# Kernel tuning notes

Hardware: AMD Instinct MI355X
Metric: run time of the kernel (lower is better)

Reference implementation:

```python
import jax, jax.numpy as jnp
import numpy as np

NEG_SLOPE = 0.1

def lrelu(x):
    return jnp.where(x >= 0, x, NEG_SLOPE * x)

def conv2d(x, w, b, padding=0, dilation=1):
    y = jax.lax.conv_general_dilated(
        x, w, window_strides=(1, 1),
        padding=[(padding, padding), (padding, padding)],
        rhs_dilation=(dilation, dilation),
        dimension_numbers=('NCHW', 'OIHW', 'NCHW'))
    return y + b[None, :, None, None]

def res_aspp(x, p):
    r1 = lrelu(conv2d(x, p['a1_w'], p['a1_b'], padding=1, dilation=1))
    r2 = lrelu(conv2d(x, p['a2_w'], p['a2_b'], padding=2, dilation=2))
    r3 = lrelu(conv2d(x, p['a3_w'], p['a3_b'], padding=4, dilation=4))
    r = conv2d(jnp.concatenate((r1, r2, r3), axis=1), p['ar_w'], p['ar_b'])
    return x + r

def deform_conv2d(x, offset, w, b):
    # x: [B,C,H,W], offset: [B,2*K,H,W] torchvision layout (y,x) per 3x3 tap
    B, C, H, W = x.shape
    KH = KW = 3
    K = KH * KW
    pad = 1
    off = offset.reshape(B, K, 2, H, W)
    ky, kx = jnp.meshgrid(jnp.arange(KH), jnp.arange(KW), indexing='ij')
    ky = ky.reshape(K).astype(x.dtype)
    kx = kx.reshape(K).astype(x.dtype)
    hh = jnp.arange(H, dtype=x.dtype)
    ww = jnp.arange(W, dtype=x.dtype)
    # sampling positions [B,K,H,W]
    py = off[:, :, 0] + (hh[None, None, :, None] - pad + ky[None, :, None, None])
    px = off[:, :, 1] + (ww[None, None, None, :] - pad + kx[None, :, None, None])
    y0 = jnp.floor(py)
    x0 = jnp.floor(px)
    wy = (py - y0)[:, None]  # [B,1,K,H,W]
    wx = (px - x0)[:, None]
    y0i = y0.astype(jnp.int32)
    x0i = x0.astype(jnp.int32)
    x_flat = x.reshape(B, C, H * W)

    def gather(iy, ix):
        valid = ((iy >= 0) & (iy < H) & (ix >= 0) & (ix < W)).astype(x.dtype)
        idx = jnp.clip(iy, 0, H - 1) * W + jnp.clip(ix, 0, W - 1)  # [B,K,H,W]
        v = jax.vmap(lambda xb, ib: xb[:, ib])(x_flat, idx.reshape(B, -1))
        return v.reshape(B, C, K, H, W) * valid[:, None]

    samp = (gather(y0i, x0i) * (1 - wy) * (1 - wx)
            + gather(y0i, x0i + 1) * (1 - wy) * wx
            + gather(y0i + 1, x0i) * wy * (1 - wx)
            + gather(y0i + 1, x0i + 1) * wy * wx)
    out = jnp.einsum('bckhw,ock->bohw', samp, w.reshape(w.shape[0], C, K))
    return out + b[None, :, None, None]

def setup_inputs() -> dict:
    key = jax.random.key(0)
    ks = jax.random.split(key, 16)
    B, C, H, W = 4, 64, 160, 160
    Cout = 64
    s = 0.05
    d = {
        'in_aux': jax.random.normal(ks[0], (B, C, H, W), jnp.float32),
        'in_ref': jax.random.normal(ks[1], (B, C, H, W), jnp.float32),
        'w01': jax.random.normal(ks[2], (Cout, 2 * C, 1, 1), jnp.float32) * s,
        'b01': jnp.zeros((Cout,), jnp.float32),
        'a1_w': jax.random.normal(ks[3], (Cout, Cout, 3, 3), jnp.float32) * s,
        'a1_b': jnp.zeros((Cout,), jnp.float32),
        'a2_w': jax.random.normal(ks[4], (Cout, Cout, 3, 3), jnp.float32) * s,
        'a2_b': jnp.zeros((Cout,), jnp.float32),
        'a3_w': jax.random.normal(ks[5], (Cout, Cout, 3, 3), jnp.float32) * s,
        'a3_b': jnp.zeros((Cout,), jnp.float32),
        'ar_w': jax.random.normal(ks[6], (Cout, 3 * Cout, 1, 1), jnp.float32) * s,
        'ar_b': jnp.zeros((Cout,), jnp.float32),
        'w02': jax.random.normal(ks[7], (18, Cout, 1, 1), jnp.float32) * s,
        'b02': jnp.zeros((18,), jnp.float32),
        'dw': jax.random.normal(ks[8], (Cout, C, 3, 3), jnp.float32) * s,
        'db': jnp.zeros((Cout,), jnp.float32),
    }
    return d

def reference(in_aux, in_ref, w01, b01, a1_w, a1_b, a2_w, a2_b, a3_w, a3_b,
              ar_w, ar_b, w02, b02, dw, db):
    cat_x = jnp.concatenate((in_aux, in_ref), axis=1)
    off_x = lrelu(conv2d(cat_x, w01, b01))
    p = {'a1_w': a1_w, 'a1_b': a1_b, 'a2_w': a2_w, 'a2_b': a2_b,
         'a3_w': a3_w, 'a3_b': a3_b, 'ar_w': ar_w, 'ar_b': ar_b}
    off_x = res_aspp(off_x, p)
    off_x = conv2d(off_x, w02, b02)
    return deform_conv2d(in_aux, off_x, dw, db)
```

## Files before the change

kernel.cpp:

```cpp
#include <hip/hip_runtime.h>
#include <math.h>

static constexpr int B = 4, H = 160, W = 160;
static constexpr int HW = H * W;
static constexpr int CHW = 64 * HW;
static constexpr int NELEM = B * CHW;

typedef short bf16x8 __attribute__((ext_vector_type(8)));
typedef float f32x4 __attribute__((ext_vector_type(4)));

__device__ __forceinline__ float lrelu(float v) { return v >= 0.f ? v : 0.1f * v; }

__device__ __forceinline__ unsigned short f2bf(float f) {
  unsigned u = __float_as_uint(f);
  return (unsigned short)((u + 0x7FFFu + ((u >> 16) & 1u)) >> 16);
}
__device__ __forceinline__ float bf2f(short u) {
  return __uint_as_float(((unsigned)(unsigned short)u) << 16);
}

__global__ __launch_bounds__(256) void k_transform(
    const float* __restrict__ w01, const float* __restrict__ dw,
    const float* __restrict__ arw, const float* __restrict__ a1w,
    const float* __restrict__ a2w, const float* __restrict__ a3w,
    float* __restrict__ wt01, unsigned short* __restrict__ wb_bf,
    unsigned short* __restrict__ wd_bf, unsigned short* __restrict__ arw_bf) {
  int i = blockIdx.x * 256 + threadIdx.x;
  if (i < 8192) {
    int ci = i >> 6, o = i & 63;
    wt01[i] = w01[o * 128 + ci];
  } else if (i < 118784) {
    int j = i - 8192;
    int ci = j & 63, co = (j >> 6) & 63;
    int kk = j >> 12;
    int dsel = kk / 9; kk -= dsel * 9;
    const float* src = dsel == 0 ? a1w : dsel == 1 ? a2w : a3w;
    wb_bf[j] = f2bf(src[(co * 64 + ci) * 9 + kk]);
  } else if (i < 155648) {
    int j = i - 118784;
    int ci = j & 63, co = (j >> 6) & 63, k = j >> 12;
    wd_bf[j] = f2bf(dw[(co * 64 + ci) * 9 + k]);
  } else if (i < 167936) {
    int j = i - 155648;
    arw_bf[j] = f2bf(arw[j]);
  }
}

__global__ __launch_bounds__(256) void k_conv1x1_in(
    const float* __restrict__ aux, const float* __restrict__ ref,
    const float* __restrict__ wt01, const float* __restrict__ b01,
    float* __restrict__ out, unsigned short* __restrict__ out_bf,
    unsigned short* __restrict__ x_bf) {
  __shared__ float s[128 * 64];
  int pos0 = blockIdx.x * 64;
  int b = pos0 / HW;
  int hw0 = pos0 - b * HW;
  int tid = threadIdx.x;
  for (int i = tid; i < 8192; i += 256) {
    int ci = i >> 6, p = i & 63;
    const float* src = (ci < 64) ? (aux + b * CHW + ci * HW)
                                 : (ref + b * CHW + (ci - 64) * HW);
    s[i] = src[hw0 + p];
  }
  __syncthreads();
  int p = tid & 63;
  int g = __builtin_amdgcn_readfirstlane(tid >> 6);
  const float* wp = wt01 + g * 16;
  float acc[16];
#pragma unroll
  for (int j = 0; j < 16; ++j) acc[j] = 0.f;
#pragma unroll 4
  for (int ci = 0; ci < 128; ++ci) {
    float sv = s[ci * 64 + p];
    const float* wrow = wp + ci * 64;
#pragma unroll
    for (int j = 0; j < 16; ++j) acc[j] += sv * wrow[j];
  }
  const float* bb = b01 + g * 16;
  int obase = (b * 64 + g * 16) * HW + hw0 + p;
  unsigned short tb[16];
#pragma unroll
  for (int j = 0; j < 16; ++j) {
    float v = lrelu(acc[j] + bb[j]);
    out[obase + j * HW] = v;
    tb[j] = f2bf(v);
  }
  unsigned short* dst = out_bf + ((size_t)(b * HW + hw0 + p)) * 64 + g * 16;
  *(uint4*)dst = *(const uint4*)&tb[0];
  *(uint4*)(dst + 8) = *(const uint4*)&tb[8];
  unsigned short xb[16];
#pragma unroll
  for (int j = 0; j < 16; ++j) xb[j] = f2bf(s[(g * 16 + j) * 64 + p]);
  unsigned short* xdst = x_bf + ((size_t)(b * HW + hw0 + p)) * 64 + g * 16;
  *(uint4*)xdst = *(const uint4*)&xb[0];
  *(uint4*)(xdst + 8) = *(const uint4*)&xb[8];
}

__global__ __launch_bounds__(256) void k_aspp3_mfma(
    const unsigned short* __restrict__ off0_bf,
    const unsigned short* __restrict__ wb_bf,
    const float* __restrict__ a1b, const float* __restrict__ a2b,
    const float* __restrict__ a3b, unsigned short* __restrict__ r_bf) {
  __shared__ unsigned short sin[576 * 40];
  int bx = blockIdx.x, by = blockIdx.y;
  int dsel = blockIdx.z >> 2, b = blockIdx.z & 3;
  int d = 1 << dsel;
  const float* bias = dsel == 0 ? a1b : dsel == 1 ? a2b : a3b;
  int tid = threadIdx.x;
  int lane = tid & 63, wid = tid >> 6;
  int m = lane & 15, q = lane >> 4;
  f32x4 acc[4][4] = {};
  const unsigned short* wbase = wb_bf + dsel * 9 * 4096;

  for (int ch = 0; ch < 2; ++ch) {
    __syncthreads();
    for (int i = tid; i < 2304; i += 256) {
      int pix = i >> 2, sub = i & 3;
      int py = pix / 24, px = pix - py * 24;
      int gy = by * 16 + py - 4, gx = bx * 16 + px - 4;
      uint4 v = make_uint4(0u, 0u, 0u, 0u);
      if (gy >= 0 && gy < H && gx >= 0 && gx < W)
        v = *(const uint4*)(off0_bf +
                            ((size_t)(b * HW + gy * W + gx)) * 64 + ch * 32 + sub * 8);
      *(uint4*)(sin + pix * 40 + sub * 8) = v;
    }
    __syncthreads();
#pragma unroll
    for (int k = 0; k < 9; ++k) {
      int ky = k / 3, kx = k - ky * 3;
      bf16x8 bfrag[4];
#pragma unroll
      for (int t = 0; t < 4; ++t)
        bfrag[t] = *(const bf16x8*)(wbase + ((k * 64 + t * 16 + m) * 64) + ch * 32 + q * 8);
      bf16x8 afrag[4];
#pragma unroll
      for (int mt = 0; mt < 4; ++mt) {
        int row = 4 + wid * 4 + mt + (ky - 1) * d;
        int col = 4 + m + (kx - 1) * d;
        afrag[mt] = *(const bf16x8*)(sin + (row * 24 + col) * 40 + q * 8);
      }
#pragma unroll
      for (int mt = 0; mt < 4; ++mt)
#pragma unroll
        for (int t = 0; t < 4; ++t)
          acc[mt][t] = __builtin_amdgcn_mfma_f32_16x16x32_bf16(
              afrag[mt], bfrag[t], acc[mt][t], 0, 0, 0);
    }
  }

  unsigned short* epb = sin;
  __syncthreads();
#pragma unroll
  for (int t = 0; t < 4; ++t) {
    float bi = bias[t * 16 + m];
#pragma unroll
    for (int mt = 0; mt < 4; ++mt) {
      int prow = wid * 4 + mt;
#pragma unroll
      for (int r = 0; r < 4; ++r) {
        int pix = prow * 16 + q * 4 + r;
        epb[pix * 72 + t * 16 + m] = f2bf(lrelu(acc[mt][t][r] + bi));
      }
    }
  }
  __syncthreads();
  {
    int pix = tid;
    int prow = pix >> 4, pcol = pix & 15;
    unsigned short* dst =
        r_bf + ((size_t)(b * HW + (by * 16 + prow) * W + bx * 16 + pcol)) * 192 +
        dsel * 64;
    const unsigned short* src = epb + pix * 72;
#pragma unroll
    for (int c = 0; c < 8; ++c)
      *(uint4*)(dst + c * 8) = *(const uint4*)(src + c * 8);
  }
}

__global__ __launch_bounds__(256) void k_merge_head_mfma(
    const unsigned short* __restrict__ r_bf, const float* __restrict__ off0,
    const unsigned short* __restrict__ arw_bf, const float* __restrict__ arb,
    const float* __restrict__ w02, const float* __restrict__ b02,
    float* __restrict__ offs) {
  __shared__ unsigned short sa[64 * 200];
  int pos0 = blockIdx.x * 64;
  int b = pos0 / HW;
  int hw0 = pos0 - b * HW;
  int tid = threadIdx.x;
  const unsigned short* gsrc = r_bf + (size_t)(b * HW + hw0) * 192;
  for (int i = tid; i < 1536; i += 256) {
    int pos = i / 24, c8 = i - pos * 24;
    *(uint4*)(sa + pos * 200 + c8 * 8) = *(const uint4*)(gsrc + i * 8);
  }
  __syncthreads();
  int lane = tid & 63, wid = tid >> 6;
  int m = lane & 15, q = lane >> 4;
  f32x4 acc[4] = {};
#pragma unroll
  for (int kc = 0; kc < 6; ++kc) {
    bf16x8 bfrag = *(const bf16x8*)(arw_bf + (wid * 16 + m) * 192 + kc * 32 + q * 8);
#pragma unroll
    for (int mt = 0; mt < 4; ++mt) {
      bf16x8 afrag = *(const bf16x8*)(sa + (mt * 16 + m) * 200 + kc * 32 + q * 8);
      acc[mt] = __builtin_amdgcn_mfma_f32_16x16x32_bf16(afrag, bfrag, acc[mt],
                                                        0, 0, 0);
    }
  }
  __syncthreads();
  float* ep = (float*)sa;
  int co = wid * 16 + m;
  float bi = arb[co];
  const float* resrow = off0 + (size_t)(b * 64 + co) * HW + hw0;
#pragma unroll
  for (int mt = 0; mt < 4; ++mt)
#pragma unroll
    for (int r = 0; r < 4; ++r) {
      int pos = mt * 16 + q * 4 + r;
      ep[pos * 65 + co] = acc[mt][r] + bi + resrow[pos];
    }
  __syncthreads();
  for (int i = tid; i < 1152; i += 256) {
    int t = i >> 6, p = i & 63;
    const float* w2 = w02 + t * 64;
    float o = b02[t];
#pragma unroll 8
    for (int c = 0; c < 64; ++c) o += ep[p * 65 + c] * w2[c];
    offs[(b * 18 + t) * HW + hw0 + p] = o;
  }
}

__global__ __launch_bounds__(256) void k_deform_mfma(
    const unsigned short* __restrict__ x_bf, const float* __restrict__ offs,
    const unsigned short* __restrict__ wd_bf, const float* __restrict__ db,
    float* __restrict__ out) {
  constexpr int SP = 72;
  __shared__ unsigned short sb[2][64 * SP];
  int blk = (blockIdx.x & 7) * 200 + (blockIdx.x >> 3);
  int pos0 = blk * 64;
  int b = pos0 / HW;
  int hw0 = pos0 - b * HW;
  int tid = threadIdx.x;
  int lane = tid & 63, wid = tid >> 6;
  int m = lane & 15, q = lane >> 4;
  int p = lane;
  int cg = wid;
  int hw = hw0 + p;
  int h = hw / W, wv = hw - h * W;
  const unsigned short* xb = x_bf + (size_t)b * HW * 64;
  const float* ob = offs + b * 18 * HW + hw;
  float offv[18];
#pragma unroll
  for (int j = 0; j < 18; ++j) offv[j] = ob[j * HW];
  f32x4 acc[4] = {};

#pragma unroll
  for (int k = 0; k < 9; ++k) {
    const int ky = k / 3, kx = k - ky * 3;
    float py = offv[2 * k] + (float)(h - 1 + ky);
    float px = offv[2 * k + 1] + (float)(wv - 1 + kx);
    float fy = floorf(py), fx = floorf(px);
    int iy0 = (int)fy, ix0 = (int)fx;
    float wy = py - fy, wx = px - fx;
    int iy1 = iy0 + 1, ix1 = ix0 + 1;
    float vy0 = (iy0 >= 0 && iy0 < H) ? 1.f : 0.f;
    float vy1 = (iy1 >= 0 && iy1 < H) ? 1.f : 0.f;
    float vx0 = (ix0 >= 0 && ix0 < W) ? 1.f : 0.f;
    float vx1 = (ix1 >= 0 && ix1 < W) ? 1.f : 0.f;
    int cy0 = min(max(iy0, 0), H - 1), cy1 = min(max(iy1, 0), H - 1);
    int cx0 = min(max(ix0, 0), W - 1), cx1 = min(max(ix1, 0), W - 1);
    float c00 = vy0 * vx0 * (1.f - wy) * (1.f - wx);
    float c01 = vy0 * vx1 * (1.f - wy) * wx;
    float c10 = vy1 * vx0 * wy * (1.f - wx);
    float c11 = vy1 * vx1 * wy * wx;
    const unsigned short* p00 = xb + (size_t)(cy0 * W + cx0) * 64 + cg * 16;
    const unsigned short* p01 = xb + (size_t)(cy0 * W + cx1) * 64 + cg * 16;
    const unsigned short* p10 = xb + (size_t)(cy1 * W + cx0) * 64 + cg * 16;
    const unsigned short* p11 = xb + (size_t)(cy1 * W + cx1) * 64 + cg * 16;
    unsigned short tb[16];
#pragma unroll
    for (int c2 = 0; c2 < 2; ++c2) {
      bf16x8 v00 = *(const bf16x8*)(p00 + c2 * 8);
      bf16x8 v01 = *(const bf16x8*)(p01 + c2 * 8);
      bf16x8 v10 = *(const bf16x8*)(p10 + c2 * 8);
      bf16x8 v11 = *(const bf16x8*)(p11 + c2 * 8);
#pragma unroll
      for (int j = 0; j < 8; ++j) {
        float sv = c00 * bf2f(v00[j]) + c01 * bf2f(v01[j]) +
                   c10 * bf2f(v10[j]) + c11 * bf2f(v11[j]);
        tb[c2 * 8 + j] = f2bf(sv);
      }
    }
    unsigned short* wr = &sb[k & 1][p * SP + cg * 16];
    *(uint4*)wr = *(const uint4*)&tb[0];
    *(uint4*)(wr + 8) = *(const uint4*)&tb[8];
    __syncthreads();
    const unsigned short* rb = &sb[k & 1][0];
#pragma unroll
    for (int kc = 0; kc < 2; ++kc) {
      bf16x8 bfrag =
          *(const bf16x8*)(wd_bf + (k * 64 + wid * 16 + m) * 64 + kc * 32 + q * 8);
#pragma unroll
      for (int mt = 0; mt < 4; ++mt) {
        bf16x8 afrag = *(const bf16x8*)(rb + (mt * 16 + m) * SP + kc * 32 + q * 8);
        acc[mt] = __builtin_amdgcn_mfma_f32_16x16x32_bf16(afrag, bfrag, acc[mt],
                                                          0, 0, 0);
      }
    }
  }
  int co = wid * 16 + m;
  float bias = db[co];
  size_t orow = (size_t)(b * 64 + co) * HW + hw0;
#pragma unroll
  for (int mt = 0; mt < 4; ++mt)
#pragma unroll
    for (int r = 0; r < 4; ++r)
      out[orow + mt * 16 + q * 4 + r] = acc[mt][r] + bias;
}

extern "C" void kernel_launch(void* const* d_in, const int* in_sizes, int n_in,
                              void* d_out, int out_size, void* d_ws, size_t ws_size,
                              hipStream_t stream) {
  const float* aux = (const float*)d_in[0];
  const float* ref = (const float*)d_in[1];
  const float* w01 = (const float*)d_in[2];
  const float* b01 = (const float*)d_in[3];
  const float* a1w = (const float*)d_in[4];
  const float* a1b = (const float*)d_in[5];
  const float* a2w = (const float*)d_in[6];
  const float* a2b = (const float*)d_in[7];
  const float* a3w = (const float*)d_in[8];
  const float* a3b = (const float*)d_in[9];
  const float* arw = (const float*)d_in[10];
  const float* arb = (const float*)d_in[11];
  const float* w02 = (const float*)d_in[12];
  const float* b02 = (const float*)d_in[13];
  const float* dw  = (const float*)d_in[14];
  const float* db  = (const float*)d_in[15];
  float* out = (float*)d_out;

  float* off0 = (float*)d_ws;
  float* offs = off0 + NELEM;
  float* wt01 = offs + B * 18 * HW;
  unsigned short* off0_bf = (unsigned short*)(wt01 + 8192);
  unsigned short* x_bf   = off0_bf + (size_t)NELEM;
  unsigned short* wb_bf  = x_bf + (size_t)NELEM;
  unsigned short* wd_bf  = wb_bf + 110592;
  unsigned short* arw_bf = wd_bf + 36864;
  unsigned short* r_bf   = arw_bf + 12288;

  k_transform<<<656, 256, 0, stream>>>(w01, dw, arw, a1w, a2w, a3w,
                                       wt01, wb_bf, wd_bf, arw_bf);
  k_conv1x1_in<<<B * HW / 64, 256, 0, stream>>>(aux, ref, wt01, b01, off0,
                                                off0_bf, x_bf);
  k_aspp3_mfma<<<dim3(10, 10, 12), 256, 0, stream>>>(
      off0_bf, wb_bf, a1b, a2b, a3b, r_bf);
  k_merge_head_mfma<<<B * HW / 64, 256, 0, stream>>>(
      r_bf, off0, arw_bf, arb, w02, b02, offs);
  k_deform_mfma<<<B * HW / 64, 256, 0, stream>>>(x_bf, offs, wd_bf, db, out);
}
```

Baseline: 334.8 us.

## Fuse three dilated ASPP branches into one block sharing a single input halo tile

The ASPP kernel now computes all three dilation branches in one block over a 16x8 pixel tile, loading the 64-channel halo tile into LDS once instead of once per branch per channel half. This removes the repeated global loads of the input halo and the extra syncs, and the output tile is written as full 192-channel rows. In exchange, each block holds three accumulator sets, grid parallelism drops to 800 blocks, and a launch_bounds occupancy hint is added. The LDS padding also changes to stride 68.

```diff
diff --git a/kernel.cpp b/kernel.cpp
--- a/kernel.cpp
+++ b/kernel.cpp
@@ -96,83 +96,92 @@
   *(uint4*)(xdst + 8) = *(const uint4*)&xb[8];
 }
 
-__global__ __launch_bounds__(256) void k_aspp3_mfma(
+__global__ __launch_bounds__(256, 2) void k_aspp3_mfma(
     const unsigned short* __restrict__ off0_bf,
     const unsigned short* __restrict__ wb_bf,
     const float* __restrict__ a1b, const float* __restrict__ a2b,
     const float* __restrict__ a3b, unsigned short* __restrict__ r_bf) {
-  __shared__ unsigned short sin[576 * 40];
-  int bx = blockIdx.x, by = blockIdx.y;
-  int dsel = blockIdx.z >> 2, b = blockIdx.z & 3;
-  int d = 1 << dsel;
-  const float* bias = dsel == 0 ? a1b : dsel == 1 ? a2b : a3b;
+  __shared__ unsigned short sin[384 * 68];
+  int bx = blockIdx.x, by = blockIdx.y, b = blockIdx.z;
   int tid = threadIdx.x;
   int lane = tid & 63, wid = tid >> 6;
   int m = lane & 15, q = lane >> 4;
-  f32x4 acc[4][4] = {};
-  const unsigned short* wbase = wb_bf + dsel * 9 * 4096;
-
-  for (int ch = 0; ch < 2; ++ch) {
-    __syncthreads();
-    for (int i = tid; i < 2304; i += 256) {
-      int pix = i >> 2, sub = i & 3;
-      int py = pix / 24, px = pix - py * 24;
-      int gy = by * 16 + py - 4, gx = bx * 16 + px - 4;
-      uint4 v = make_uint4(0u, 0u, 0u, 0u);
-      if (gy >= 0 && gy < H && gx >= 0 && gx < W)
-        v = *(const uint4*)(off0_bf +
-                            ((size_t)(b * HW + gy * W + gx)) * 64 + ch * 32 + sub * 8);
-      *(uint4*)(sin + pix * 40 + sub * 8) = v;
-    }
-    __syncthreads();
+
+  for (int i = tid; i < 3072; i += 256) {
+    int pix = i >> 3, sub = i & 7;
+    int py = pix / 24, px = pix - py * 24;
+    int gy = by * 8 + py - 4, gx = bx * 16 + px - 4;
+    uint4 v = make_uint4(0u, 0u, 0u, 0u);
+    if (gy >= 0 && gy < H && gx >= 0 && gx < W)
+      v = *(const uint4*)(off0_bf +
+                          ((size_t)(b * HW + gy * W + gx)) * 64 + sub * 8);
+    *(uint4*)(sin + pix * 68 + sub * 8) = v;
+  }
+  __syncthreads();
+
+  f32x4 acc[3][2][4] = {};
+#pragma unroll
+  for (int dsel = 0; dsel < 3; ++dsel) {
+    const int d = 1 << dsel;
+    const unsigned short* wbase = wb_bf + dsel * 9 * 4096;
 #pragma unroll
     for (int k = 0; k < 9; ++k) {
       int ky = k / 3, kx = k - ky * 3;
-      bf16x8 bfrag[4];
-#pragma unroll
-      for (int t = 0; t < 4; ++t)
-        bfrag[t] = *(const bf16x8*)(wbase + ((k * 64 + t * 16 + m) * 64) + ch * 32 + q * 8);
-      bf16x8 afrag[4];
-#pragma unroll
-      for (int mt = 0; mt < 4; ++mt) {
-        int row = 4 + wid * 4 + mt + (ky - 1) * d;
-        int col = 4 + m + (kx - 1) * d;
-        afrag[mt] = *(const bf16x8*)(sin + (row * 24 + col) * 40 + q * 8);
+#pragma unroll
+      for (int cih = 0; cih < 2; ++cih) {
+        bf16x8 bfrag[4];
+#pragma unroll
+        for (int t = 0; t < 4; ++t)
+          bfrag[t] = *(const bf16x8*)(wbase + (k * 64 + t * 16 + m) * 64 +
+                                      cih * 32 + q * 8);
+        bf16x8 afrag[2];
+#pragma unroll
+        for (int mt = 0; mt < 2; ++mt) {
+          int row = 4 + wid * 2 + mt + (ky - 1) * d;
+          int col = 4 + m + (kx - 1) * d;
+          afrag[mt] = *(const bf16x8*)(sin + (row * 24 + col) * 68 +
+                                       cih * 32 + q * 8);
+        }
+#pragma unroll
+        for (int mt = 0; mt < 2; ++mt)
+#pragma unroll
+          for (int t = 0; t < 4; ++t)
+            acc[dsel][mt][t] = __builtin_amdgcn_mfma_f32_16x16x32_bf16(
+                afrag[mt], bfrag[t], acc[dsel][mt][t], 0, 0, 0);
       }
-#pragma unroll
-      for (int mt = 0; mt < 4; ++mt)
-#pragma unroll
-        for (int t = 0; t < 4; ++t)
-          acc[mt][t] = __builtin_amdgcn_mfma_f32_16x16x32_bf16(
-              afrag[mt], bfrag[t], acc[mt][t], 0, 0, 0);
-    }
-  }
-
+    }
+  }
+
+  __syncthreads();
   unsigned short* epb = sin;
-  __syncthreads();
-#pragma unroll
-  for (int t = 0; t < 4; ++t) {
-    float bi = bias[t * 16 + m];
-#pragma unroll
-    for (int mt = 0; mt < 4; ++mt) {
-      int prow = wid * 4 + mt;
-#pragma unroll
-      for (int r = 0; r < 4; ++r) {
-        int pix = prow * 16 + q * 4 + r;
-        epb[pix * 72 + t * 16 + m] = f2bf(lrelu(acc[mt][t][r] + bi));
+#pragma unroll
+  for (int dsel = 0; dsel < 3; ++dsel) {
+    const float* bias = dsel == 0 ? a1b : dsel == 1 ? a2b : a3b;
+#pragma unroll
+    for (int t = 0; t < 4; ++t) {
+      float bi = bias[t * 16 + m];
+#pragma unroll
+      for (int mt = 0; mt < 2; ++mt) {
+        int prow = wid * 2 + mt;
+#pragma unroll
+        for (int r = 0; r < 4; ++r) {
+          int pix = prow * 16 + q * 4 + r;
+          epb[pix * 200 + dsel * 64 + t * 16 + m] =
+              f2bf(lrelu(acc[dsel][mt][t][r] + bi));
+        }
       }
     }
   }
   __syncthreads();
   {
-    int pix = tid;
+    int pix = tid >> 1, half = tid & 1;
     int prow = pix >> 4, pcol = pix & 15;
     unsigned short* dst =
-        r_bf + ((size_t)(b * HW + (by * 16 + prow) * W + bx * 16 + pcol)) * 192 +
-        dsel * 64;
-    const unsigned short* src = epb + pix * 72;
-#pragma unroll
-    for (int c = 0; c < 8; ++c)
+        r_bf + ((size_t)(b * HW + (by * 8 + prow) * W + bx * 16 + pcol)) * 192 +
+        half * 96;
+    const unsigned short* src = epb + pix * 200 + half * 96;
+#pragma unroll
+    for (int c = 0; c < 12; ++c)
       *(uint4*)(dst + c * 8) = *(const uint4*)(src + c * 8);
   }
 }
@@ -352,7 +361,7 @@
                                        wt01, wb_bf, wd_bf, arw_bf);
   k_conv1x1_in<<<B * HW / 64, 256, 0, stream>>>(aux, ref, wt01, b01, off0,
                                                 off0_bf, x_bf);
-  k_aspp3_mfma<<<dim3(10, 10, 12), 256, 0, stream>>>(
+  k_aspp3_mfma<<<dim3(10, 20, 4), 256, 0, stream>>>(
       off0_bf, wb_bf, a1b, a2b, a3b, r_bf);
   k_merge_head_mfma<<<B * HW / 64, 256, 0, stream>>>(
       r_bf, off0, arw_bf, arb, w02, b02, offs);
```

Result: slower. 373.0 us (+11.4%).

## Load ASPP conv operands directly from global per wave, drop shared halo tile

Applied to the files above, without the earlier changes.

The dilated 3x3 ASPP kernel no longer stages a 24x24 halo tile in shared memory. Each wave now owns 64 linear pixels and fetches its A fragments straight from global memory (through cache), masking taps that fall outside the image. The grid is flattened to 1200 blocks with a swizzled mapping so that consecutive hardware slots land on different work groups, and shared memory is kept only for a per-wave epilogue transpose. This removes the staging barriers and the halo-load overhead, at the cost of redundant global/L2 reads of neighbouring pixels across the 9 taps.

```diff
diff --git a/kernel.cpp b/kernel.cpp
--- a/kernel.cpp
+++ b/kernel.cpp
@@ -101,80 +101,82 @@
     const unsigned short* __restrict__ wb_bf,
     const float* __restrict__ a1b, const float* __restrict__ a2b,
     const float* __restrict__ a3b, unsigned short* __restrict__ r_bf) {
-  __shared__ unsigned short sin[576 * 40];
-  int bx = blockIdx.x, by = blockIdx.y;
-  int dsel = blockIdx.z >> 2, b = blockIdx.z & 3;
-  int d = 1 << dsel;
-  const float* bias = dsel == 0 ? a1b : dsel == 1 ? a2b : a3b;
+  __shared__ unsigned short ep[4][64 * 68];
   int tid = threadIdx.x;
   int lane = tid & 63, wid = tid >> 6;
   int m = lane & 15, q = lane >> 4;
+  int blk = (blockIdx.x & 7) * 150 + (blockIdx.x >> 3);
+  int wg = __builtin_amdgcn_readfirstlane(blk * 4 + wid);
+  int dsel = wg / 1600;
+  int rem = wg - dsel * 1600;
+  int b = rem / 400;
+  int g = rem - b * 400;
+  int px0 = g * 64;
+  const int d = 1 << dsel;
+  const unsigned short* xb = off0_bf + (size_t)b * HW * 64;
+  const unsigned short* wbase = wb_bf + dsel * 36864;
+  const float* bias = dsel == 0 ? a1b : dsel == 1 ? a2b : a3b;
+
+  int hwp[4], hp[4], wp[4];
+#pragma unroll
+  for (int mt = 0; mt < 4; ++mt) {
+    hwp[mt] = px0 + mt * 16 + m;
+    hp[mt] = hwp[mt] / W;
+    wp[mt] = hwp[mt] - hp[mt] * W;
+  }
+
   f32x4 acc[4][4] = {};
-  const unsigned short* wbase = wb_bf + dsel * 9 * 4096;
-
-  for (int ch = 0; ch < 2; ++ch) {
-    __syncthreads();
-    for (int i = tid; i < 2304; i += 256) {
-      int pix = i >> 2, sub = i & 3;
-      int py = pix / 24, px = pix - py * 24;
-      int gy = by * 16 + py - 4, gx = bx * 16 + px - 4;
-      uint4 v = make_uint4(0u, 0u, 0u, 0u);
-      if (gy >= 0 && gy < H && gx >= 0 && gx < W)
-        v = *(const uint4*)(off0_bf +
-                            ((size_t)(b * HW + gy * W + gx)) * 64 + ch * 32 + sub * 8);
-      *(uint4*)(sin + pix * 40 + sub * 8) = v;
-    }
-    __syncthreads();
-#pragma unroll
-    for (int k = 0; k < 9; ++k) {
-      int ky = k / 3, kx = k - ky * 3;
+#pragma unroll
+  for (int k = 0; k < 9; ++k) {
+    const int ky = k / 3, kx = k - ky * 3;
+    int dy = (ky - 1) * d, dx = (kx - 1) * d;
+    int kofs = dy * W + dx;
+    bool va[4];
+    int at[4];
+#pragma unroll
+    for (int mt = 0; mt < 4; ++mt) {
+      va[mt] = ((unsigned)(hp[mt] + dy) < (unsigned)H) &
+               ((unsigned)(wp[mt] + dx) < (unsigned)W);
+      at[mt] = hwp[mt] + kofs;
+    }
+#pragma unroll
+    for (int cih = 0; cih < 2; ++cih) {
       bf16x8 bfrag[4];
 #pragma unroll
       for (int t = 0; t < 4; ++t)
-        bfrag[t] = *(const bf16x8*)(wbase + ((k * 64 + t * 16 + m) * 64) + ch * 32 + q * 8);
-      bf16x8 afrag[4];
+        bfrag[t] = *(const bf16x8*)(wbase + (k * 64 + t * 16 + m) * 64 +
+                                    cih * 32 + q * 8);
 #pragma unroll
       for (int mt = 0; mt < 4; ++mt) {
-        int row = 4 + wid * 4 + mt + (ky - 1) * d;
-        int col = 4 + m + (kx - 1) * d;
-        afrag[mt] = *(const bf16x8*)(sin + (row * 24 + col) * 40 + q * 8);
-      }
-#pragma unroll
-      for (int mt = 0; mt < 4; ++mt)
+        bf16x8 af = {0, 0, 0, 0, 0, 0, 0, 0};
+        if (va[mt])
+          af = *(const bf16x8*)(xb + (size_t)at[mt] * 64 + cih * 32 + q * 8);
 #pragma unroll
         for (int t = 0; t < 4; ++t)
           acc[mt][t] = __builtin_amdgcn_mfma_f32_16x16x32_bf16(
-              afrag[mt], bfrag[t], acc[mt][t], 0, 0, 0);
-    }
-  }
-
-  unsigned short* epb = sin;
-  __syncthreads();
+              af, bfrag[t], acc[mt][t], 0, 0, 0);
+      }
+    }
+  }
+
+  unsigned short* e = ep[wid];
 #pragma unroll
   for (int t = 0; t < 4; ++t) {
     float bi = bias[t * 16 + m];
 #pragma unroll
-    for (int mt = 0; mt < 4; ++mt) {
-      int prow = wid * 4 + mt;
-#pragma unroll
-      for (int r = 0; r < 4; ++r) {
-        int pix = prow * 16 + q * 4 + r;
-        epb[pix * 72 + t * 16 + m] = f2bf(lrelu(acc[mt][t][r] + bi));
-      }
-    }
-  }
-  __syncthreads();
-  {
-    int pix = tid;
-    int prow = pix >> 4, pcol = pix & 15;
-    unsigned short* dst =
-        r_bf + ((size_t)(b * HW + (by * 16 + prow) * W + bx * 16 + pcol)) * 192 +
-        dsel * 64;
-    const unsigned short* src = epb + pix * 72;
-#pragma unroll
-    for (int c = 0; c < 8; ++c)
-      *(uint4*)(dst + c * 8) = *(const uint4*)(src + c * 8);
-  }
+    for (int mt = 0; mt < 4; ++mt)
+#pragma unroll
+      for (int r = 0; r < 4; ++r)
+        e[(mt * 16 + q * 4 + r) * 68 + t * 16 + m] =
+            f2bf(lrelu(acc[mt][t][r] + bi));
+  }
+  __syncthreads();
+  unsigned short* dst =
+      r_bf + ((size_t)(b * HW + px0 + lane)) * 192 + dsel * 64;
+  const unsigned short* src = e + lane * 68;
+#pragma unroll
+  for (int c = 0; c < 8; ++c)
+    *(uint4*)(dst + c * 8) = *(const uint4*)(src + c * 8);
 }
 
 __global__ __launch_bounds__(256) void k_merge_head_mfma(
@@ -352,8 +354,7 @@
                                        wt01, wb_bf, wd_bf, arw_bf);
   k_conv1x1_in<<<B * HW / 64, 256, 0, stream>>>(aux, ref, wt01, b01, off0,
                                                 off0_bf, x_bf);
-  k_aspp3_mfma<<<dim3(10, 10, 12), 256, 0, stream>>>(
-      off0_bf, wb_bf, a1b, a2b, a3b, r_bf);
+  k_aspp3_mfma<<<1200, 256, 0, stream>>>(off0_bf, wb_bf, a1b, a2b, a3b, r_bf);
   k_merge_head_mfma<<<B * HW / 64, 256, 0, stream>>>(
       r_bf, off0, arw_bf, arb, w02, b02, offs);
   k_deform_mfma<<<B * HW / 64, 256, 0, stream>>>(x_bf, offs, wd_bf, db, out);
```

After: 368.7 us. 1.1x slower.

## Use zero-padded bf16 activation layout and direct-to-LDS loads in ASPP conv

Applied to the files above, without the earlier changes.

The bf16 conv input is now stored in a zero-padded 168x168 layout with guard rows, so every dilated tap becomes a contiguous 256-pixel slab loaded with global_load_lds. This replaces the bounds-checked halo staging. The ASPP kernel becomes a flat 1D grid over padded-row tiles with XCD-aware block remapping that keeps the three dilations of a tile on the same die. The costs are extra computation on padding pixels, a zero-fill pass over the padded buffer in the transform kernel, and a sync plus reload per tap.

```diff
diff --git a/kernel.cpp b/kernel.cpp
--- a/kernel.cpp
+++ b/kernel.cpp
@@ -6,6 +6,13 @@
 static constexpr int CHW = 64 * HW;
 static constexpr int NELEM = B * CHW;
 
+static constexpr int WP = 168;
+static constexpr int HP = 168;
+static constexpr int PHW = WP * HP;
+static constexpr int PGUARD = 704;
+static constexpr int PSTRIDE = 30720;
+static constexpr int IMGOFS = PGUARD + 4 * WP + 4;
+
 typedef short bf16x8 __attribute__((ext_vector_type(8)));
 typedef float f32x4 __attribute__((ext_vector_type(4)));
 
@@ -17,6 +24,12 @@
 }
 __device__ __forceinline__ float bf2f(short u) {
   return __uint_as_float(((unsigned)(unsigned short)u) << 16);
+}
+
+__device__ __forceinline__ void glds16(const unsigned short* g, unsigned short* l) {
+  __builtin_amdgcn_global_load_lds(
+      (const __attribute__((address_space(1))) void*)g,
+      (__attribute__((address_space(3))) void*)l, 16, 0, 0);
 }
 
 __global__ __launch_bounds__(256) void k_transform(
@@ -24,8 +37,15 @@
     const float* __restrict__ arw, const float* __restrict__ a1w,
     const float* __restrict__ a2w, const float* __restrict__ a3w,
     float* __restrict__ wt01, unsigned short* __restrict__ wb_bf,
-    unsigned short* __restrict__ wd_bf, unsigned short* __restrict__ arw_bf) {
+    unsigned short* __restrict__ wd_bf, unsigned short* __restrict__ arw_bf,
+    unsigned short* __restrict__ off0p) {
   int i = blockIdx.x * 256 + threadIdx.x;
+  uint4* zp = (uint4*)off0p;
+#pragma unroll
+  for (int j = 0; j < 6; ++j) {
+    unsigned u = (unsigned)i + (unsigned)j * 167936u;
+    if (u < 983040u) zp[u] = make_uint4(0u, 0u, 0u, 0u);
+  }
   if (i < 8192) {
     int ci = i >> 6, o = i & 63;
     wt01[i] = w01[o * 128 + ci];
@@ -49,7 +69,7 @@
 __global__ __launch_bounds__(256) void k_conv1x1_in(
     const float* __restrict__ aux, const float* __restrict__ ref,
     const float* __restrict__ wt01, const float* __restrict__ b01,
-    float* __restrict__ out, unsigned short* __restrict__ out_bf,
+    float* __restrict__ out, unsigned short* __restrict__ off0p,
     unsigned short* __restrict__ x_bf) {
   __shared__ float s[128 * 64];
   int pos0 = blockIdx.x * 64;
@@ -85,7 +105,10 @@
     out[obase + j * HW] = v;
     tb[j] = f2bf(v);
   }
-  unsigned short* dst = out_bf + ((size_t)(b * HW + hw0 + p)) * 64 + g * 16;
+  int hw = hw0 + p;
+  int h = hw / W, w = hw - h * W;
+  unsigned short* dst =
+      off0p + ((size_t)b * PSTRIDE + IMGOFS + h * WP + w) * 64 + g * 16;
   *(uint4*)dst = *(const uint4*)&tb[0];
   *(uint4*)(dst + 8) = *(const uint4*)&tb[8];
   unsigned short xb[16];
@@ -97,83 +120,81 @@
 }
 
 __global__ __launch_bounds__(256) void k_aspp3_mfma(
-    const unsigned short* __restrict__ off0_bf,
+    const unsigned short* __restrict__ off0p,
     const unsigned short* __restrict__ wb_bf,
     const float* __restrict__ a1b, const float* __restrict__ a2b,
     const float* __restrict__ a3b, unsigned short* __restrict__ r_bf) {
-  __shared__ unsigned short sin[576 * 40];
-  int bx = blockIdx.x, by = blockIdx.y;
-  int dsel = blockIdx.z >> 2, b = blockIdx.z & 3;
-  int d = 1 << dsel;
-  const float* bias = dsel == 0 ? a1b : dsel == 1 ? a2b : a3b;
+  __shared__ unsigned short sa[256 * 72];
   int tid = threadIdx.x;
   int lane = tid & 63, wid = tid >> 6;
   int m = lane & 15, q = lane >> 4;
+
+  int p0 = blockIdx.x;
+  int xcd = p0 & 7, ii = p0 >> 3;
+  int base = xcd < 4 ? xcd * 167 : 668 + (xcd - 4) * 166;
+  int lid = base + ii;
+  int dsel = lid % 3;
+  int tj = lid / 3;
+  int b = tj / 111;
+  int tile = tj - b * 111;
+  int pos0 = tile * 256;
+  const int d = 1 << dsel;
+  const unsigned short* pb = off0p + (size_t)b * PSTRIDE * 64;
+  const float* bias = dsel == 0 ? a1b : dsel == 1 ? a2b : a3b;
+
   f32x4 acc[4][4] = {};
-  const unsigned short* wbase = wb_bf + dsel * 9 * 4096;
-
-  for (int ch = 0; ch < 2; ++ch) {
+#pragma unroll
+  for (int k9 = 0; k9 < 9; ++k9) {
+    const int ky = k9 / 3, kx = k9 - ky * 3;
+    const int ofs = ((ky - 1) * WP + (kx - 1)) * d;
+    const unsigned short* src = pb + (size_t)(PGUARD + pos0 + ofs) * 64;
     __syncthreads();
-    for (int i = tid; i < 2304; i += 256) {
-      int pix = i >> 2, sub = i & 3;
-      int py = pix / 24, px = pix - py * 24;
-      int gy = by * 16 + py - 4, gx = bx * 16 + px - 4;
-      uint4 v = make_uint4(0u, 0u, 0u, 0u);
-      if (gy >= 0 && gy < H && gx >= 0 && gx < W)
-        v = *(const uint4*)(off0_bf +
-                            ((size_t)(b * HW + gy * W + gx)) * 64 + ch * 32 + sub * 8);
-      *(uint4*)(sin + pix * 40 + sub * 8) = v;
-    }
+#pragma unroll
+    for (int r = 0; r < 8; ++r)
+      glds16(src + r * 2048 + tid * 8, sa + r * 2048 + tid * 8);
     __syncthreads();
-#pragma unroll
-    for (int k = 0; k < 9; ++k) {
-      int ky = k / 3, kx = k - ky * 3;
+    const unsigned short* wk = wb_bf + (dsel * 9 + k9) * 4096;
+#pragma unroll
+    for (int kc = 0; kc < 2; ++kc) {
       bf16x8 bfrag[4];
 #pragma unroll
       for (int t = 0; t < 4; ++t)
-        bfrag[t] = *(const bf16x8*)(wbase + ((k * 64 + t * 16 + m) * 64) + ch * 32 + q * 8);
-      bf16x8 afrag[4];
+        bfrag[t] = *(const bf16x8*)(wk + (t * 16 + m) * 64 + kc * 32 + q * 8);
 #pragma unroll
       for (int mt = 0; mt < 4; ++mt) {
-        int row = 4 + wid * 4 + mt + (ky - 1) * d;
-        int col = 4 + m + (kx - 1) * d;
-        afrag[mt] = *(const bf16x8*)(sin + (row * 24 + col) * 40 + q * 8);
-      }
-#pragma unroll
-      for (int mt = 0; mt < 4; ++mt)
+        bf16x8 afrag =
+            *(const bf16x8*)(sa + (wid * 64 + mt * 16 + m) * 64 + kc * 32 + q * 8);
 #pragma unroll
         for (int t = 0; t < 4; ++t)
           acc[mt][t] = __builtin_amdgcn_mfma_f32_16x16x32_bf16(
-              afrag[mt], bfrag[t], acc[mt][t], 0, 0, 0);
-    }
-  }
-
-  unsigned short* epb = sin;
+              afrag, bfrag[t], acc[mt][t], 0, 0, 0);
+      }
+    }
+  }
+
   __syncthreads();
 #pragma unroll
   for (int t = 0; t < 4; ++t) {
     float bi = bias[t * 16 + m];
 #pragma unroll
-    for (int mt = 0; mt < 4; ++mt) {
-      int prow = wid * 4 + mt;
-#pragma unroll
-      for (int r = 0; r < 4; ++r) {
-        int pix = prow * 16 + q * 4 + r;
-        epb[pix * 72 + t * 16 + m] = f2bf(lrelu(acc[mt][t][r] + bi));
-      }
-    }
+    for (int mt = 0; mt < 4; ++mt)
+#pragma unroll
+      for (int r = 0; r < 4; ++r)
+        sa[(wid * 64 + mt * 16 + q * 4 + r) * 72 + t * 16 + m] =
+            f2bf(lrelu(acc[mt][t][r] + bi));
   }
   __syncthreads();
   {
-    int pix = tid;
-    int prow = pix >> 4, pcol = pix & 15;
-    unsigned short* dst =
-        r_bf + ((size_t)(b * HW + (by * 16 + prow) * W + bx * 16 + pcol)) * 192 +
-        dsel * 64;
-    const unsigned short* src = epb + pix * 72;
-#pragma unroll
-    for (int c = 0; c < 8; ++c)
-      *(uint4*)(dst + c * 8) = *(const uint4*)(src + c * 8);
+    int qa = pos0 + tid;
+    int pr = qa / WP, pc = qa - pr * WP;
+    if (pr >= 4 && pr < 164 && pc >= 4 && pc < 164) {
+      int hw = (pr - 4) * W + (pc - 4);
+      unsigned short* dst = r_bf + ((size_t)(b * HW + hw)) * 192 + dsel * 64;
+      const unsigned short* s2 = sa + tid * 72;
+#pragma unroll
+      for (int c = 0; c < 8; ++c)
+        *(uint4*)(dst + c * 8) = *(const uint4*)(s2 + c * 8);
+    }
   }
 }
 
@@ -341,19 +362,18 @@
   float* off0 = (float*)d_ws;
   float* offs = off0 + NELEM;
   float* wt01 = offs + B * 18 * HW;
-  unsigned short* off0_bf = (unsigned short*)(wt01 + 8192);
-  unsigned short* x_bf   = off0_bf + (size_t)NELEM;
+  unsigned short* off0p = (unsigned short*)(wt01 + 8192);
+  unsigned short* x_bf   = off0p + (size_t)B * PSTRIDE * 64;
   unsigned short* wb_bf  = x_bf + (size_t)NELEM;
   unsigned short* wd_bf  = wb_bf + 110592;
   unsigned short* arw_bf = wd_bf + 36864;
   unsigned short* r_bf   = arw_bf + 12288;
 
   k_transform<<<656, 256, 0, stream>>>(w01, dw, arw, a1w, a2w, a3w,
-                                       wt01, wb_bf, wd_bf, arw_bf);
+                                       wt01, wb_bf, wd_bf, arw_bf, off0p);
   k_conv1x1_in<<<B * HW / 64, 256, 0, stream>>>(aux, ref, wt01, b01, off0,
-                                                off0_bf, x_bf);
-  k_aspp3_mfma<<<dim3(10, 10, 12), 256, 0, stream>>>(
-      off0_bf, wb_bf, a1b, a2b, a3b, r_bf);
+                                                off0p, x_bf);
+  k_aspp3_mfma<<<1332, 256, 0, stream>>>(off0p, wb_bf, a1b, a2b, a3b, r_bf);
   k_merge_head_mfma<<<B * HW / 64, 256, 0, stream>>>(
       r_bf, off0, arw_bf, arb, w02, b02, offs);
   k_deform_mfma<<<B * HW / 64, 256, 0, stream>>>(x_bf, offs, wd_bf, db, out);
```

New measurement: 330.3 us. No clear change (-1.3%).
